# Kernel tuning notes

Measured on AMD Instinct MI355X. Metric: run time of the kernel, lower is better.

## Reference

```python
import jax, jax.numpy as jnp
import numpy as np

N_NODES = 800_000
N_FRAGS = 100_000
N_ROOTS = 2_000
NODE_FEATS = 86
HIDDEN = 128
MAX_BROKEN = 6
OUT_DIM = MAX_BROKEN * 2 + 1  # 13
MLP_IN = HIDDEN * 3 + OUT_DIM  # 397


def _lin_init(key, fan_in, fan_out):
    k1, k2 = jax.random.split(key)
    bound = 1.0 / np.sqrt(fan_in)
    W = jax.random.uniform(k1, (fan_in, fan_out), jnp.float32, -bound, bound)
    b = jax.random.uniform(k2, (fan_out,), jnp.float32, -bound, bound)
    return W, b


def setup_inputs() -> dict:
    key = jax.random.key(0)
    ks = jax.random.split(key, 16)
    node_h = jax.random.normal(ks[0], (N_NODES, NODE_FEATS), jnp.float32)
    segment_ids = jnp.sort(jax.random.randint(ks[1], (N_NODES,), 0, N_FRAGS))
    root_repr = jax.random.normal(ks[2], (N_ROOTS, NODE_FEATS), jnp.float32)
    ind_maps = jax.random.randint(ks[3], (N_FRAGS,), 0, N_ROOTS)
    broken = jax.random.randint(ks[4], (N_FRAGS,), 0, OUT_DIM)
    W_root, b_root = _lin_init(ks[5], NODE_FEATS, HIDDEN)
    W_in, b_in = _lin_init(ks[6], NODE_FEATS, HIDDEN)
    W_g1, b_g1 = _lin_init(ks[7], HIDDEN, HIDDEN)
    W_g2, b_g2 = _lin_init(ks[8], HIDDEN, HIDDEN)
    W_m1, b_m1 = _lin_init(ks[9], MLP_IN, HIDDEN)
    W_m2, b_m2 = _lin_init(ks[10], HIDDEN, HIDDEN)
    W_out, b_out = _lin_init(ks[11], HIDDEN, OUT_DIM)
    W_attn, b_attn = _lin_init(ks[12], HIDDEN, OUT_DIM)
    return dict(node_h=node_h, segment_ids=segment_ids, root_repr=root_repr,
                ind_maps=ind_maps, broken=broken,
                W_root=W_root, b_root=b_root, W_in=W_in, b_in=b_in,
                W_g1=W_g1, b_g1=b_g1, W_g2=W_g2, b_g2=b_g2,
                W_m1=W_m1, b_m1=b_m1, W_m2=W_m2, b_m2=b_m2,
                W_out=W_out, b_out=b_out, W_attn=W_attn, b_attn=b_attn)


def _segment_mean(x, seg_ids, num_segments):
    sums = jax.ops.segment_sum(x, seg_ids, num_segments=num_segments)
    counts = jax.ops.segment_sum(jnp.ones((x.shape[0],), x.dtype), seg_ids,
                                 num_segments=num_segments)
    return sums / jnp.maximum(counts, 1.0)[:, None]


def reference(node_h, segment_ids, root_repr, ind_maps, broken,
              W_root, b_root, W_in, b_in, W_g1, b_g1, W_g2, b_g2,
              W_m1, b_m1, W_m2, b_m2, W_out, b_out, W_attn, b_attn):
    # root encoder: Linear + ReLU (dropout=0)
    root_emb = jax.nn.relu(root_repr @ W_root + b_root)        # [R, H]
    ext_root = root_emb[ind_maps]                              # [F, H] gather
    # node input + 2 GNN (nodewise Linear+ReLU fallback) layers
    frag_h = node_h @ W_in + b_in                              # [N, H]
    frag_h = jax.nn.relu(frag_h @ W_g1 + b_g1)
    frag_h = jax.nn.relu(frag_h @ W_g2 + b_g2)
    # ragged mean-pool per fragment graph (dgl.mean_nodes)
    avg_frags = _segment_mean(frag_h, segment_ids, N_FRAGS)    # [F, H]
    # one-hot of clamped broken-bond counts
    broken_oh = jax.nn.one_hot(jnp.clip(broken, 0, MAX_BROKEN * 2), OUT_DIM,
                               dtype=frag_h.dtype)             # [F, 13]
    cat = jnp.concatenate([ext_root, ext_root - avg_frags, avg_frags,
                           broken_oh], axis=-1)                # [F, 397]
    hidden = jax.nn.relu(jax.nn.relu(cat @ W_m1 + b_m1) @ W_m2 + b_m2)
    output = jax.nn.sigmoid(hidden @ W_out + b_out)            # [F, 13]
    attn_weights = hidden @ W_attn + b_attn                    # [F, 13]
    return output, attn_weights
```

## Files before the change

kernel.cpp:

```cpp
#include <hip/hip_runtime.h>
#include <math.h>

typedef __attribute__((ext_vector_type(8))) short short8;
typedef __attribute__((ext_vector_type(4))) float float4v;

#define AST 136
#define CST 424

__device__ __forceinline__ unsigned short f2bf(float f) {
    union { float f; unsigned u; } v; v.f = f;
    return (unsigned short)((v.u + 0x7fffu + ((v.u >> 16) & 1u)) >> 16);
}
__device__ __forceinline__ float bf2f(unsigned v) {
    union { unsigned u; float f; } x; x.u = v << 16; return x.f;
}

template<int KP>
__device__ __forceinline__ void loadW(const unsigned short* __restrict__ WT,
                                      int lane, int tb, short8 Wv[2][KP / 32])
{
    const int col0 = lane & 15, q = lane >> 4;
#pragma unroll
    for (int t = 0; t < 2; ++t)
#pragma unroll
        for (int ksi = 0; ksi < KP / 32; ++ksi)
            Wv[t][ksi] = *(const short8*)(WT + (size_t)((tb + t) * 16 + col0) * KP
                                          + ksi * 32 + q * 8);
}

template<int KP, int MT>
__device__ __forceinline__ void layerP(const unsigned short* X, int astr,
                                       const float* __restrict__ bias,
                                       int lane, int tb,
                                       const short8 Wv[2][KP / 32], float4v acc[MT][2])
{
    const int col0 = lane & 15, q = lane >> 4;
#pragma unroll
    for (int t = 0; t < 2; ++t) {
        float b = bias[(tb + t) * 16 + col0];
#pragma unroll
        for (int mt = 0; mt < MT; ++mt) acc[mt][t] = (float4v){b, b, b, b};
    }
#pragma unroll
    for (int ksi = 0; ksi < KP / 32; ++ksi) {
        const int k0 = ksi * 32 + q * 8;
#pragma unroll
        for (int mt = 0; mt < MT; ++mt) {
            short8 A = *(const short8*)(X + (mt * 16 + col0) * astr + k0);
#pragma unroll
            for (int t = 0; t < 2; ++t)
                acc[mt][t] = __builtin_amdgcn_mfma_f32_16x16x32_bf16(A, Wv[t][ksi], acc[mt][t], 0, 0, 0);
        }
    }
}

template<int KP, int MT>
__device__ __forceinline__ void layerG(const unsigned short* X, int astr,
                                       const unsigned short* __restrict__ WT,
                                       const float* __restrict__ bias,
                                       int lane, int tb, float4v acc[MT][2])
{
    const int col0 = lane & 15, q = lane >> 4;
#pragma unroll
    for (int t = 0; t < 2; ++t) {
        float b = bias[(tb + t) * 16 + col0];
#pragma unroll
        for (int mt = 0; mt < MT; ++mt) acc[mt][t] = (float4v){b, b, b, b};
    }
#pragma unroll
    for (int ks = 0; ks < KP; ks += 32) {
        const int k0 = ks + q * 8;
        short8 B[2];
#pragma unroll
        for (int t = 0; t < 2; ++t)
            B[t] = *(const short8*)(WT + (size_t)((tb + t) * 16 + col0) * KP + k0);
#pragma unroll
        for (int mt = 0; mt < MT; ++mt) {
            short8 A = *(const short8*)(X + (mt * 16 + col0) * astr + k0);
#pragma unroll
            for (int t = 0; t < 2; ++t)
                acc[mt][t] = __builtin_amdgcn_mfma_f32_16x16x32_bf16(A, B[t], acc[mt][t], 0, 0, 0);
        }
    }
}

template<int MT>
__device__ __forceinline__ void storeP(float4v acc[MT][2], unsigned short* Y,
                                       int lane, int tb, bool relu)
{
    const int col0 = lane & 15, q = lane >> 4;
#pragma unroll
    for (int mt = 0; mt < MT; ++mt)
#pragma unroll
        for (int t = 0; t < 2; ++t)
#pragma unroll
            for (int r = 0; r < 4; ++r) {
                float v = acc[mt][t][r];
                if (relu) v = fmaxf(v, 0.0f);
                Y[(mt * 16 + q * 4 + r) * AST + (tb + t) * 16 + col0] = f2bf(v);
            }
}

__global__ void prep_kernel(const float* __restrict__ W_in, const float* __restrict__ W_g1,
                            const float* __restrict__ W_g2, const float* __restrict__ W_m1,
                            const float* __restrict__ W_m2, const float* __restrict__ W_out,
                            const float* __restrict__ W_attn, unsigned short* __restrict__ wt)
{
    int i = blockIdx.x * 256 + threadIdx.x;
    unsigned short* WT_in = wt;
    unsigned short* WT_g1 = WT_in + 12288;
    unsigned short* WT_g2 = WT_g1 + 16384;
    unsigned short* WT_m1 = WT_g2 + 16384;
    unsigned short* WT_m2 = WT_m1 + 53248;
    unsigned short* WT_h  = WT_m2 + 16384;
    if (i < 12288) { int n = i / 96, k = i - n * 96;
        WT_in[i] = (k < 86) ? f2bf(W_in[k * 128 + n]) : 0; return; }
    i -= 12288;
    if (i < 16384) { int n = i >> 7, k = i & 127;
        WT_g1[i] = f2bf(W_g1[k * 128 + n]); return; }
    i -= 16384;
    if (i < 16384) { int n = i >> 7, k = i & 127;
        WT_g2[i] = f2bf(W_g2[k * 128 + n]); return; }
    i -= 16384;
    if (i < 53248) { int n = i / 416, k = i - n * 416;
        WT_m1[i] = (k < 397) ? f2bf(W_m1[k * 128 + n]) : 0; return; }
    i -= 53248;
    if (i < 16384) { int n = i >> 7, k = i & 127;
        WT_m2[i] = f2bf(W_m2[k * 128 + n]); return; }
    i -= 16384;
    if (i < 4096) { int n = i >> 7, k = i & 127;
        WT_h[i] = (n < 13) ? f2bf(W_out[k * 13 + n])
                           : (n < 26 ? f2bf(W_attn[k * 13 + (n - 13)]) : 0); }
}

__global__ void root_kernel(const float* __restrict__ root_repr,
                            const float* __restrict__ W_root,
                            const float* __restrict__ b_root,
                            float* __restrict__ root_emb)
{
    __shared__ float x[86];
    const int r = blockIdx.x, tid = threadIdx.x;
    if (tid < 86) x[tid] = root_repr[(size_t)r * 86 + tid];
    __syncthreads();
    float acc = b_root[tid];
    for (int k = 0; k < 86; ++k)
        acc = fmaf(x[k], W_root[k * 128 + tid], acc);
    root_emb[(size_t)r * 128 + tid] = fmaxf(acc, 0.0f);
}

__global__ __launch_bounds__(256, 4)
void node_kernel(const float* __restrict__ node_h, const int* __restrict__ seg_ids,
                 const unsigned short* __restrict__ WT_in, const float* __restrict__ b_in,
                 const unsigned short* __restrict__ WT_g1, const float* __restrict__ b_g1,
                 const unsigned short* __restrict__ WT_g2, const float* __restrict__ b_g2,
                 float* __restrict__ frag_sum, float* __restrict__ frag_cnt)
{
    __shared__ __align__(16) unsigned short X[64 * AST];
    __shared__ __align__(16) unsigned short Y[64 * AST];
    __shared__ int segs[64];
    const int tid = threadIdx.x, wv = tid >> 6, lane = tid & 63, tb = wv * 2;
    const long n0 = (long)blockIdx.x * 64;

    short8 W1[2][3];
    loadW<96>(WT_in, lane, tb, W1);

    if (tid < 64) segs[tid] = seg_ids[n0 + tid];
    {
        const float4* src = (const float4*)(node_h + n0 * 86);
#pragma unroll
        for (int j = 0; j < 6; ++j) {
            int i4 = j * 256 + tid;
            if (i4 < 1376) {
                float4 v = src[i4];
                int e = i4 << 2;
                int n = e / 86, k = e - n * 86;
                X[n * AST + k] = f2bf(v.x);
                int e1 = e + 1; n = e1 / 86; k = e1 - n * 86; X[n * AST + k] = f2bf(v.y);
                int e2 = e + 2; n = e2 / 86; k = e2 - n * 86; X[n * AST + k] = f2bf(v.z);
                int e3 = e + 3; n = e3 / 86; k = e3 - n * 86; X[n * AST + k] = f2bf(v.w);
            }
        }
        for (int idx = tid; idx < 640; idx += 256) {
            int n = idx / 10, k = idx - n * 10;
            X[n * AST + 86 + k] = 0;
        }
    }
    __syncthreads();

    float4v acc[4][2];
    layerP<96, 4>(X, AST, b_in, lane, tb, W1, acc);
    short8 W2[2][4];
    loadW<128>(WT_g1, lane, tb, W2);
    storeP<4>(acc, Y, lane, tb, false);
    __syncthreads();
    layerP<128, 4>(Y, AST, b_g1, lane, tb, W2, acc);
    short8 W3[2][4];
    loadW<128>(WT_g2, lane, tb, W3);
    storeP<4>(acc, X, lane, tb, true);
    __syncthreads();
    layerP<128, 4>(X, AST, b_g2, lane, tb, W3, acc);
    storeP<4>(acc, Y, lane, tb, true);
    __syncthreads();

    {
        const int col = tid & 127, half = tid >> 7, r0 = half << 5;
        const int prevSeg = (half == 1) ? segs[31] : -1;
        const int nextSeg = (half == 0) ? segs[32] : -1;
        int cur = segs[r0], runStart = r0;
        float sum = 0.f, cnt = 0.f;
        for (int n = r0; n < r0 + 32; ++n) {
            int s = segs[n];
            if (s != cur) {
                bool bnd = (runStart == r0) && (half == 0 || prevSeg == cur);
                if (bnd) atomicAdd(&frag_sum[(size_t)cur * 128 + col], sum);
                else     frag_sum[(size_t)cur * 128 + col] = sum;
                if (col == 0) {
                    if (bnd) atomicAdd(&frag_cnt[cur], cnt);
                    else     frag_cnt[cur] = cnt;
                }
                sum = 0.f; cnt = 0.f; cur = s; runStart = n;
            }
            sum += bf2f((unsigned)Y[n * AST + col]);
            cnt += 1.f;
        }
        bool bnd = ((runStart == r0) && (half == 0 || prevSeg == cur))
                   || (half == 1) || (nextSeg == cur);
        if (bnd) atomicAdd(&frag_sum[(size_t)cur * 128 + col], sum);
        else     frag_sum[(size_t)cur * 128 + col] = sum;
        if (col == 0) {
            if (bnd) atomicAdd(&frag_cnt[cur], cnt);
            else     frag_cnt[cur] = cnt;
        }
    }
}

__global__ __launch_bounds__(256, 4)
void frag_kernel(const float* __restrict__ root_emb, const float* __restrict__ frag_sum,
                 const float* __restrict__ frag_cnt, const int* __restrict__ ind_maps,
                 const int* __restrict__ broken,
                 const unsigned short* __restrict__ WT_m1, const float* __restrict__ b_m1,
                 const unsigned short* __restrict__ WT_m2, const float* __restrict__ b_m2,
                 const unsigned short* __restrict__ WT_h,
                 const float* __restrict__ b_out, const float* __restrict__ b_attn,
                 float* __restrict__ out0, float* __restrict__ out1)
{
    __shared__ __align__(16) unsigned short cat[32 * CST];
    __shared__ __align__(16) unsigned short Y[32 * AST];
    unsigned short* X2 = cat;
    const int tid = threadIdx.x, wv = tid >> 6, lane = tid & 63, tb = wv * 2;
    const int col0 = lane & 15, q = lane >> 4;
    const long f0 = (long)blockIdx.x * 32;

    {
        const int m = tid >> 3, j = tid & 7;
        int fc = (int)f0 + m; if (fc > 99999) fc = 99999;
        const int rid = ind_maps[fc];
        const float inv = 1.0f / fmaxf(frag_cnt[fc], 1.0f);
        unsigned short* row = cat + m * CST;
#pragma unroll
        for (int jj = 0; jj < 4; ++jj) {
            int k = j * 16 + jj * 4;
            float4 e = *(const float4*)(root_emb + (size_t)rid * 128 + k);
            float4 s = *(const float4*)(frag_sum + (size_t)fc * 128 + k);
            float sx = s.x * inv, sy = s.y * inv, sz = s.z * inv, sw = s.w * inv;
            uint2 w;
            w.x = (unsigned)f2bf(e.x) | ((unsigned)f2bf(e.y) << 16);
            w.y = (unsigned)f2bf(e.z) | ((unsigned)f2bf(e.w) << 16);
            *(uint2*)(row + k) = w;
            w.x = (unsigned)f2bf(e.x - sx) | ((unsigned)f2bf(e.y - sy) << 16);
            w.y = (unsigned)f2bf(e.z - sz) | ((unsigned)f2bf(e.w - sw) << 16);
            *(uint2*)(row + 128 + k) = w;
            w.x = (unsigned)f2bf(sx) | ((unsigned)f2bf(sy) << 16);
            w.y = (unsigned)f2bf(sz) | ((unsigned)f2bf(sw) << 16);
            *(uint2*)(row + 256 + k) = w;
        }
        if (j == 7) {
            int b = broken[fc]; b = b < 0 ? 0 : (b > 12 ? 12 : b);
#pragma unroll
            for (int kk = 0; kk < 32; kk += 4) {
                uint2 w;
                w.x = ((kk     == b) ? 0x3f80u : 0u) | (((kk + 1 == b) ? 0x3f80u : 0u) << 16);
                w.y = ((kk + 2 == b) ? 0x3f80u : 0u) | (((kk + 3 == b) ? 0x3f80u : 0u) << 16);
                *(uint2*)(row + 384 + kk) = w;
            }
        }
    }
    __syncthreads();

    float4v acc[2][2];
    layerG<416, 2>(cat, CST, WT_m1, b_m1, lane, tb, acc);
    short8 Wm2[2][4];
    loadW<128>(WT_m2, lane, tb, Wm2);
    storeP<2>(acc, Y, lane, tb, true);
    __syncthreads();
    layerP<128, 2>(Y, AST, b_m2, lane, tb, Wm2, acc);
    const int mrow = wv & 1, t_h = wv >> 1;
    short8 Wh[4];
#pragma unroll
    for (int ksi = 0; ksi < 4; ++ksi)
        Wh[ksi] = *(const short8*)(WT_h + (t_h * 16 + col0) * 128 + ksi * 32 + q * 8);
    storeP<2>(acc, X2, lane, tb, true);
    __syncthreads();

    {
        const int cc = t_h * 16 + col0;
        float b = cc < 13 ? b_out[cc] : (cc < 26 ? b_attn[cc - 13] : 0.0f);
        float4v hacc = (float4v){b, b, b, b};
#pragma unroll
        for (int ksi = 0; ksi < 4; ++ksi) {
            short8 A = *(const short8*)(X2 + (mrow * 16 + col0) * AST + ksi * 32 + q * 8);
            hacc = __builtin_amdgcn_mfma_f32_16x16x32_bf16(A, Wh[ksi], hacc, 0, 0, 0);
        }
#pragma unroll
        for (int r = 0; r < 4; ++r) {
            long ff = f0 + mrow * 16 + q * 4 + r;
            if (ff < 100000) {
                float v = hacc[r];
                if (cc < 13)      out0[ff * 13 + cc] = 1.0f / (1.0f + expf(-v));
                else if (cc < 26) out1[ff * 13 + cc - 13] = v;
            }
        }
    }
}

extern "C" void kernel_launch(void* const* d_in, const int* in_sizes, int n_in,
                              void* d_out, int out_size, void* d_ws, size_t ws_size,
                              hipStream_t stream)
{
    const float* node_h    = (const float*)d_in[0];
    const int*   seg_ids   = (const int*)d_in[1];
    const float* root_repr = (const float*)d_in[2];
    const int*   ind_maps  = (const int*)d_in[3];
    const int*   broken    = (const int*)d_in[4];
    const float* W_root = (const float*)d_in[5];  const float* b_root = (const float*)d_in[6];
    const float* W_in   = (const float*)d_in[7];  const float* b_in   = (const float*)d_in[8];
    const float* W_g1   = (const float*)d_in[9];  const float* b_g1   = (const float*)d_in[10];
    const float* W_g2   = (const float*)d_in[11]; const float* b_g2   = (const float*)d_in[12];
    const float* W_m1   = (const float*)d_in[13]; const float* b_m1   = (const float*)d_in[14];
    const float* W_m2   = (const float*)d_in[15]; const float* b_m2   = (const float*)d_in[16];
    const float* W_out  = (const float*)d_in[17]; const float* b_out  = (const float*)d_in[18];
    const float* W_attn = (const float*)d_in[19]; const float* b_attn = (const float*)d_in[20];

    char* ws = (char*)d_ws;
    float* root_emb = (float*)ws;
    float* frag_sum = (float*)(ws + 1024000);
    float* frag_cnt = (float*)(ws + 52224000);
    unsigned short* wt = (unsigned short*)(ws + 52624000);
    const unsigned short* WT_in = wt;
    const unsigned short* WT_g1 = wt + 12288;
    const unsigned short* WT_g2 = WT_g1 + 16384;
    const unsigned short* WT_m1 = WT_g2 + 16384;
    const unsigned short* WT_m2 = WT_m1 + 53248;
    const unsigned short* WT_h  = WT_m2 + 16384;

    hipMemsetAsync(frag_sum, 0, 51600000, stream);

    float* out0 = (float*)d_out;
    float* out1 = out0 + (size_t)100000 * 13;

    prep_kernel<<<464, 256, 0, stream>>>(W_in, W_g1, W_g2, W_m1, W_m2, W_out, W_attn, wt);
    root_kernel<<<2000, 128, 0, stream>>>(root_repr, W_root, b_root, root_emb);
    node_kernel<<<12500, 256, 0, stream>>>(node_h, seg_ids, WT_in, b_in,
                                           WT_g1, b_g1, WT_g2, b_g2, frag_sum, frag_cnt);
    frag_kernel<<<3125, 256, 0, stream>>>(root_emb, frag_sum, frag_cnt, ind_maps, broken,
                                          WT_m1, b_m1, WT_m2, b_m2, WT_h, b_out, b_attn,
                                          out0, out1);
}
```

Before: 591.2 us.

## Keep node MLP activations in registers via transposed MFMA and lane shuffles

The node kernel now gives each wave its own 16 rows and computes the transposed product (weights as the A operand, activations as B), so each layer's output can be repacked into the next layer's input fragments with wave shuffles instead of round-tripping through shared memory with block barriers. Node features are loaded straight from global memory into register fragments, and weights are streamed from global/L2 per MFMA rather than preloaded. The fragment kernel reuses part of the cat buffer instead of a separate Y buffer, which cuts LDS use but needs extra barriers. The cost is more weight loads per wave, plus higher register pressure from the 8 accumulator tiles and the shuffle temporaries.

```diff
diff --git a/kernel.cpp b/kernel.cpp
--- a/kernel.cpp
+++ b/kernel.cpp
@@ -13,6 +13,67 @@
 }
 __device__ __forceinline__ float bf2f(unsigned v) {
     union { unsigned u; float f; } x; x.u = v << 16; return x.f;
+}
+__device__ __forceinline__ unsigned shflu(unsigned v, int srcLane) {
+    return (unsigned)__shfl((int)v, srcLane, 64);
+}
+__device__ __forceinline__ uint2 pack4(float4v a, bool relu) {
+    float v0 = a[0], v1 = a[1], v2 = a[2], v3 = a[3];
+    if (relu) { v0 = fmaxf(v0, 0.f); v1 = fmaxf(v1, 0.f);
+                v2 = fmaxf(v2, 0.f); v3 = fmaxf(v3, 0.f); }
+    uint2 w;
+    w.x = (unsigned)f2bf(v0) | ((unsigned)f2bf(v1) << 16);
+    w.y = (unsigned)f2bf(v2) | ((unsigned)f2bf(v3) << 16);
+    return w;
+}
+
+template<int KP>
+__device__ __forceinline__ void layerR(const unsigned short* __restrict__ WT,
+                                       const float* __restrict__ bias,
+                                       int lane, const short8 Xv[KP / 32],
+                                       float4v acc[8])
+{
+    const int c = lane & 15, q = lane >> 4;
+#pragma unroll
+    for (int nt = 0; nt < 8; ++nt) {
+        float4 b4 = *(const float4*)(bias + nt * 16 + q * 4);
+        acc[nt] = (float4v){b4.x, b4.y, b4.z, b4.w};
+    }
+#pragma unroll
+    for (int nt = 0; nt < 8; ++nt)
+#pragma unroll
+        for (int ks = 0; ks < KP / 32; ++ks) {
+            short8 Wv = *(const short8*)(WT + (size_t)(nt * 16 + c) * KP + ks * 32 + q * 8);
+            acc[nt] = __builtin_amdgcn_mfma_f32_16x16x32_bf16(Wv, Xv[ks], acc[nt], 0, 0, 0);
+        }
+}
+
+template<bool RELU>
+__device__ __forceinline__ void transitionR(const float4v acc[8], int lane,
+                                            short8 Xv[4])
+{
+    const int c = lane & 15, q = lane >> 4;
+    const int sl = c + 16 * ((2 * q) & 3);
+    const int sh = c + 16 * ((2 * q + 1) & 3);
+    uint2 P[8];
+#pragma unroll
+    for (int nt = 0; nt < 8; ++nt) P[nt] = pack4(acc[nt], RELU);
+    uint2 L[8], H[8];
+#pragma unroll
+    for (int nt = 0; nt < 8; ++nt) {
+        L[nt].x = shflu(P[nt].x, sl); L[nt].y = shflu(P[nt].y, sl);
+        H[nt].x = shflu(P[nt].x, sh); H[nt].y = shflu(P[nt].y, sh);
+    }
+    const bool lo = (q < 2);
+#pragma unroll
+    for (int ks = 0; ks < 4; ++ks) {
+        union { unsigned u[4]; short8 s; } un;
+        un.u[0] = lo ? L[2 * ks].x : L[2 * ks + 1].x;
+        un.u[1] = lo ? L[2 * ks].y : L[2 * ks + 1].y;
+        un.u[2] = lo ? H[2 * ks].x : H[2 * ks + 1].x;
+        un.u[3] = lo ? H[2 * ks].y : H[2 * ks + 1].y;
+        Xv[ks] = un.s;
+    }
 }
 
 template<int KP>
@@ -155,51 +216,44 @@
                  const unsigned short* __restrict__ WT_g2, const float* __restrict__ b_g2,
                  float* __restrict__ frag_sum, float* __restrict__ frag_cnt)
 {
-    __shared__ __align__(16) unsigned short X[64 * AST];
-    __shared__ __align__(16) unsigned short Y[64 * AST];
+    __shared__ __align__(16) unsigned short H3[64 * AST];
     __shared__ int segs[64];
-    const int tid = threadIdx.x, wv = tid >> 6, lane = tid & 63, tb = wv * 2;
+    const int tid = threadIdx.x, wv = tid >> 6, lane = tid & 63;
+    const int c = lane & 15, q = lane >> 4;
     const long n0 = (long)blockIdx.x * 64;
 
-    short8 W1[2][3];
-    loadW<96>(WT_in, lane, tb, W1);
-
     if (tid < 64) segs[tid] = seg_ids[n0 + tid];
+
+    short8 Xv1[3];
     {
-        const float4* src = (const float4*)(node_h + n0 * 86);
-#pragma unroll
-        for (int j = 0; j < 6; ++j) {
-            int i4 = j * 256 + tid;
-            if (i4 < 1376) {
-                float4 v = src[i4];
-                int e = i4 << 2;
-                int n = e / 86, k = e - n * 86;
-                X[n * AST + k] = f2bf(v.x);
-                int e1 = e + 1; n = e1 / 86; k = e1 - n * 86; X[n * AST + k] = f2bf(v.y);
-                int e2 = e + 2; n = e2 / 86; k = e2 - n * 86; X[n * AST + k] = f2bf(v.z);
-                int e3 = e + 3; n = e3 / 86; k = e3 - n * 86; X[n * AST + k] = f2bf(v.w);
+        const float* xrow = node_h + (size_t)(n0 + wv * 16 + c) * 86;
+#pragma unroll
+        for (int ks = 0; ks < 3; ++ks) {
+            union { unsigned u[4]; short8 s; } un;
+#pragma unroll
+            for (int p = 0; p < 4; ++p) {
+                int e = ks * 32 + q * 8 + p * 2;
+                float a0 = 0.f, a1 = 0.f;
+                if (e < 86) { float2 f = *(const float2*)(xrow + e); a0 = f.x; a1 = f.y; }
+                un.u[p] = (unsigned)f2bf(a0) | ((unsigned)f2bf(a1) << 16);
             }
-        }
-        for (int idx = tid; idx < 640; idx += 256) {
-            int n = idx / 10, k = idx - n * 10;
-            X[n * AST + 86 + k] = 0;
-        }
-    }
-    __syncthreads();
-
-    float4v acc[4][2];
-    layerP<96, 4>(X, AST, b_in, lane, tb, W1, acc);
-    short8 W2[2][4];
-    loadW<128>(WT_g1, lane, tb, W2);
-    storeP<4>(acc, Y, lane, tb, false);
-    __syncthreads();
-    layerP<128, 4>(Y, AST, b_g1, lane, tb, W2, acc);
-    short8 W3[2][4];
-    loadW<128>(WT_g2, lane, tb, W3);
-    storeP<4>(acc, X, lane, tb, true);
-    __syncthreads();
-    layerP<128, 4>(X, AST, b_g2, lane, tb, W3, acc);
-    storeP<4>(acc, Y, lane, tb, true);
+            Xv1[ks] = un.s;
+        }
+    }
+
+    float4v acc[8];
+    layerR<96>(WT_in, b_in, lane, Xv1, acc);
+    short8 Xv[4];
+    transitionR<false>(acc, lane, Xv);
+    layerR<128>(WT_g1, b_g1, lane, Xv, acc);
+    transitionR<true>(acc, lane, Xv);
+    layerR<128>(WT_g2, b_g2, lane, Xv, acc);
+
+#pragma unroll
+    for (int nt = 0; nt < 8; ++nt) {
+        uint2 w2 = pack4(acc[nt], true);
+        *(uint2*)(H3 + (wv * 16 + c) * AST + nt * 16 + q * 4) = w2;
+    }
     __syncthreads();
 
     {
@@ -220,7 +274,7 @@
                 }
                 sum = 0.f; cnt = 0.f; cur = s; runStart = n;
             }
-            sum += bf2f((unsigned)Y[n * AST + col]);
+            sum += bf2f((unsigned)H3[n * AST + col]);
             cnt += 1.f;
         }
         bool bnd = ((runStart == r0) && (half == 0 || prevSeg == cur))
@@ -245,7 +299,7 @@
                  float* __restrict__ out0, float* __restrict__ out1)
 {
     __shared__ __align__(16) unsigned short cat[32 * CST];
-    __shared__ __align__(16) unsigned short Y[32 * AST];
+    unsigned short* H1 = cat + 32 * AST;
     unsigned short* X2 = cat;
     const int tid = threadIdx.x, wv = tid >> 6, lane = tid & 63, tb = wv * 2;
     const int col0 = lane & 15, q = lane >> 4;
@@ -291,14 +345,16 @@
     layerG<416, 2>(cat, CST, WT_m1, b_m1, lane, tb, acc);
     short8 Wm2[2][4];
     loadW<128>(WT_m2, lane, tb, Wm2);
-    storeP<2>(acc, Y, lane, tb, true);
-    __syncthreads();
-    layerP<128, 2>(Y, AST, b_m2, lane, tb, Wm2, acc);
+    __syncthreads();
+    storeP<2>(acc, H1, lane, tb, true);
+    __syncthreads();
+    layerP<128, 2>(H1, AST, b_m2, lane, tb, Wm2, acc);
     const int mrow = wv & 1, t_h = wv >> 1;
     short8 Wh[4];
 #pragma unroll
     for (int ksi = 0; ksi < 4; ++ksi)
         Wh[ksi] = *(const short8*)(WT_h + (t_h * 16 + col0) * 128 + ksi * 32 + q * 8);
+    __syncthreads();
     storeP<2>(acc, X2, lane, tb, true);
     __syncthreads();
 
```

Result: slower. 867.1 us (+46.7%).
